# Kernel optimization log

Measured on AMD Instinct MI355X. Metric: run time of the kernel, lower is better.

## Reference

```python
import jax, jax.numpy as jnp
import numpy as np

B, T, N, F_IN = 8, 16, 1000, 16
E = 16000
H, D = 4, 32          # heads, gat_hidden_shape
HL = 64               # lstm hidden
OUT = 8
NEG_SLOPE = 0.2       # PyG GATConv default


def setup_inputs() -> dict:
    key = jax.random.key(0)
    ks = jax.random.split(key, 10)
    def init(k, shape, fan):
        return (jax.random.normal(k, shape, jnp.float32) / np.sqrt(fan)).astype(jnp.float32)
    x = jax.random.normal(ks[0], (B, T, N, F_IN), jnp.float32)
    edge_index = jax.random.randint(ks[1], (2, E), 0, N)
    W_gat = init(ks[2], (F_IN, H * D), F_IN)       # GATConv lin weight
    att_src = init(ks[3], (H, D), D)
    att_dst = init(ks[4], (H, D), D)
    b_gat = jnp.zeros((H * D,), jnp.float32)
    W_ih = init(ks[5], (4 * HL, H * D), H * D)     # LSTM, gate order i,f,g,o
    W_hh = init(ks[6], (4 * HL, HL), HL)
    b_ih = jnp.zeros((4 * HL,), jnp.float32)
    b_hh = jnp.zeros((4 * HL,), jnp.float32)
    W_clf = init(ks[7], (OUT, HL), HL)
    b_clf = jnp.zeros((OUT,), jnp.float32)
    return {"x": x, "edge_index": edge_index, "W_gat": W_gat, "att_src": att_src,
            "att_dst": att_dst, "b_gat": b_gat, "W_ih": W_ih, "W_hh": W_hh,
            "b_ih": b_ih, "b_hh": b_hh, "W_clf": W_clf, "b_clf": b_clf}


def reference(x, edge_index, W_gat, att_src, att_dst, b_gat,
              W_ih, W_hh, b_ih, b_hh, W_clf, b_clf):
    Bx, Tx, Nx, Fx = x.shape
    x_flat = x.reshape(Bx * Tx, Nx, Fx)
    # PyG GATConv adds self-loops by default
    loop = jnp.arange(Nx)
    src = jnp.concatenate([edge_index[0], loop])
    dst = jnp.concatenate([edge_index[1], loop])

    def gat_graph(xg):  # xg: [N, F]
        xp = (xg @ W_gat).reshape(Nx, H, D)                 # [N,H,D]
        a_s = jnp.einsum('nhd,hd->nh', xp, att_src)         # [N,H]
        a_d = jnp.einsum('nhd,hd->nh', xp, att_dst)
        e = jax.nn.leaky_relu(a_s[src] + a_d[dst], NEG_SLOPE)  # [E+N,H]
        m = jax.ops.segment_max(e, dst, num_segments=Nx)       # per-target softmax
        ex = jnp.exp(e - m[dst])
        denom = jax.ops.segment_sum(ex, dst, num_segments=Nx)
        alpha = ex / denom[dst]                                # [E+N,H]
        out = jax.ops.segment_sum(alpha[..., None] * xp[src], dst, num_segments=Nx)
        return out.reshape(Nx, H * D) + b_gat                  # [N, H*D]

    gat = jax.vmap(gat_graph)(x_flat)          # [B*T, N, H*D]
    gat = jax.nn.relu(gat)
    pooled = gat.max(axis=1)                   # global_max_pool -> [B*T, H*D]
    seq = pooled.reshape(Bx, Tx, H * D)

    h0 = jnp.zeros((Bx, HL), jnp.float32)
    c0 = jnp.zeros((Bx, HL), jnp.float32)

    def step(carry, xt):  # xt: [B, H*D]
        h, c = carry
        gates = xt @ W_ih.T + h @ W_hh.T + b_ih + b_hh
        i, f, g, o = jnp.split(gates, 4, axis=-1)
        i, f, o = jax.nn.sigmoid(i), jax.nn.sigmoid(f), jax.nn.sigmoid(o)
        g = jnp.tanh(g)
        c = f * c + i * g
        h = o * jnp.tanh(c)
        return (h, c), None

    (hT, _), _ = jax.lax.scan(step, (h0, c0), seq.transpose(1, 0, 2))
    return hT @ W_clf.T + b_clf                # [B, OUT]
```

## Files before the change

### kernel.cpp

```cpp
#include <hip/hip_runtime.h>
#include <hip/hip_bf16.h>
#include <stdint.h>

namespace {
constexpr int kB = 8, kT = 16, kN = 1000, kF = 16;
constexpr int kE = 16000;
constexpr int kH = 4, kHD = 128;
constexpr int kHL = 64, kOUT = 8;
constexpr int kG = kB * kT;
constexpr float kNeg = 0.2f;

constexpr size_t CX_WG   = 0;
constexpr size_t CX_ATS  = CX_WG   + 2048;
constexpr size_t CX_ATD  = CX_ATS  + 128;
constexpr size_t CX_BG   = CX_ATD  + 128;
constexpr size_t CX_WIH  = CX_BG   + 128;
constexpr size_t CX_WHH  = CX_WIH  + 32768;
constexpr size_t CX_BIH  = CX_WHH  + 16384;
constexpr size_t CX_BHH  = CX_BIH  + 256;
constexpr size_t CX_WCLF = CX_BHH  + 256;
constexpr size_t CX_BCLF = CX_WCLF + 512;
constexpr size_t CX_TOTAL = CX_BCLF + 8;

constexpr size_t OFF_FLAG  = 0;
constexpr size_t OFF_ROW   = 256;
constexpr size_t OFF_COL   = 4352;
constexpr size_t OFF_POOL  = 68608;
constexpr size_t OFF_CANON = 134400;
constexpr size_t OFF_AS    = 239872;
}

__device__ __forceinline__ float bf2f(unsigned short u) {
    return __uint_as_float(((uint32_t)u) << 16);
}
__device__ __forceinline__ float blo(uint32_t u) { return __uint_as_float(u << 16); }
__device__ __forceinline__ unsigned short f2bf(float f) {
    uint32_t u = __float_as_uint(f);
    uint32_t r = (u + 0x7fff + ((u >> 16) & 1)) >> 16;
    return (unsigned short)r;
}
__device__ __forceinline__ float sigm(float x) { return 1.f / (1.f + __expf(-x)); }

__device__ __forceinline__ int detect_isf(const unsigned short* xs, int t,
                                          int nthr, int* sh_cnt) {
    if (t == 0) *sh_cnt = 0;
    __syncthreads();
    int loc = 0;
    for (int i = t; i < 2048; i += nthr) {
        unsigned short u = xs[i];
        int ex = (u >> 7) & 0xff;
        if (u == 0 || (ex >= 97 && ex <= 143)) loc++;
    }
    atomicAdd(sh_cnt, loc);
    __syncthreads();
    return (*sh_cnt >= (2048 * 8) / 10) ? 0 : 1;
}

struct ConvArgs {
    const unsigned short* src[10];
    int n[10];
};

__global__ __launch_bounds__(256) void mega_setup(
        const void* __restrict__ xraw, const int* __restrict__ ei,
        ConvArgs ca,
        const unsigned short* __restrict__ WgR,
        const unsigned short* __restrict__ atsR,
        const unsigned short* __restrict__ atdR,
        int* __restrict__ flag, int* __restrict__ row, int* __restrict__ col,
        unsigned short* __restrict__ canon,
        unsigned short* __restrict__ xp_all,
        float* __restrict__ as_all, float* __restrict__ ad_all,
        unsigned int* __restrict__ pooled) {
    const int t = threadIdx.x;
    const unsigned short* xs = (const unsigned short*)xraw;

    if (blockIdx.x == 0) {
        __shared__ int cnt[1024];
        __shared__ int wtot[4];
        const int lane = t & 63, w = t >> 6;
        for (int i = t; i < 1024; i += 256) cnt[i] = 0;
        __syncthreads();
        const int* dst = ei + kE;
        for (int e = t; e < kE; e += 256) atomicAdd(&cnt[dst[e]], 1);
        __syncthreads();
        const int n0 = 4 * t;
        int c0 = cnt[n0], c1 = cnt[n0 + 1], c2 = cnt[n0 + 2], c3 = cnt[n0 + 3];
        int s0 = c0, s1 = s0 + c1, s2 = s1 + c2, s3 = s2 + c3;
        int tot = s3;
#pragma unroll
        for (int sft = 1; sft < 64; sft <<= 1) {
            int v = __shfl_up(tot, sft, 64);
            if (lane >= sft) tot += v;
        }
        if (lane == 63) wtot[w] = tot;
        __syncthreads();
        int wexcl = 0;
        for (int j = 0; j < w; ++j) wexcl += wtot[j];
        const int excl = wexcl + tot - s3;
        if (t == 0) row[0] = 0;
        if (n0 < kN) {
            row[n0 + 1] = excl + s0;
            row[n0 + 2] = excl + s1;
            row[n0 + 3] = excl + s2;
            row[n0 + 4] = excl + s3;
        }
        __syncthreads();
        cnt[n0] = excl; cnt[n0 + 1] = excl + s0;
        cnt[n0 + 2] = excl + s1; cnt[n0 + 3] = excl + s2;
        __syncthreads();
        for (int e = t; e < kE; e += 256) {
            int d0 = dst[e];
            int pos = atomicAdd(&cnt[d0], 1);
            col[pos] = ei[e];
        }
    } else if (blockIdx.x == 1) {
        __shared__ int dcnt;
        const int isf = detect_isf(xs, t, 256, &dcnt);
        if (t == 0) *flag = isf;
        size_t base = 0;
        for (int s = 0; s < 10; ++s) {
            const int n = ca.n[s];
            if (isf) {
                const float* fp = (const float*)ca.src[s];
                for (int i = t; i < n; i += 256) canon[base + i] = f2bf(fp[i]);
            } else {
                const unsigned short* sp = ca.src[s];
                for (int i = t; i < n; i += 256) canon[base + i] = sp[i];
            }
            base += (size_t)n;
        }
        for (int i = t; i < kG * kHD; i += 256) pooled[i] = 0u;
    } else {
        __shared__ int dcnt;
        __shared__ float Wl[kF * kHD];
        __shared__ float asl[kHD], adl[kHD];
        __shared__ float xr[64][kF];
        __shared__ float ws2[2][4][16];
        const int isf = detect_isf(xs, t, 256, &dcnt);
        const int i0 = blockIdx.x - 2;
        const int v = i0 & 7;
        const int jj = i0 >> 3;
        const int gl = v + 8 * (jj >> 4);
        const int nb = jj & 15;
        if (isf) {
            const float* wf = (const float*)WgR;
            for (int i = t; i < kF * kHD; i += 256) Wl[i] = wf[i];
            if (t < kHD) asl[t] = ((const float*)atsR)[t];
            else if (t < 2 * kHD) adl[t - kHD] = ((const float*)atdR)[t - kHD];
        } else {
            for (int i = t; i < kF * kHD; i += 256) Wl[i] = bf2f(WgR[i]);
            if (t < kHD) asl[t] = bf2f(atsR[t]);
            else if (t < 2 * kHD) adl[t - kHD] = bf2f(atdR[t - kHD]);
        }
        const int n0 = nb * 64;
        const int nn = min(64, kN - n0);
        const size_t xbase = (size_t)gl * kN * kF + (size_t)n0 * kF;
        if (isf) {
            const float* xf = (const float*)xraw;
            for (int i = t; i < nn * kF; i += 256) xr[i >> 4][i & 15] = xf[xbase + i];
        } else {
            for (int i = t; i < nn * kF; i += 256) xr[i >> 4][i & 15] = bf2f(xs[xbase + i]);
        }
        __syncthreads();

        if (t < 128) {
            const int sd = t >> 6, h = (t >> 4) & 3, f = t & 15;
            const float* att = sd ? adl : asl;
            float acc = 0.f;
#pragma unroll
            for (int d = 0; d < 32; ++d) acc += Wl[f * kHD + h * 32 + d] * att[h * 32 + d];
            ws2[sd][h][f] = acc;
        }

        unsigned short* xp = xp_all + (size_t)gl * kN * kHD;
        {
            const int c = t & 127;
            const int sub1 = t >> 7;
            float wreg[kF];
#pragma unroll
            for (int f = 0; f < kF; ++f) wreg[f] = Wl[f * kHD + c];
            for (int ln = sub1; ln < nn; ln += 2) {
                const float4* xrv = (const float4*)xr[ln];
                const float4 x0 = xrv[0], x1 = xrv[1], x2 = xrv[2], x3 = xrv[3];
                float vv = x0.x * wreg[0]  + x0.y * wreg[1]  + x0.z * wreg[2]  + x0.w * wreg[3]
                         + x1.x * wreg[4]  + x1.y * wreg[5]  + x1.z * wreg[6]  + x1.w * wreg[7]
                         + x2.x * wreg[8]  + x2.y * wreg[9]  + x2.z * wreg[10] + x2.w * wreg[11]
                         + x3.x * wreg[12] + x3.y * wreg[13] + x3.z * wreg[14] + x3.w * wreg[15];
                xp[(size_t)(n0 + ln) * kHD + c] = f2bf(vv);
            }
        }
        __syncthreads();

        {
            const int n = t >> 2, h = t & 3;
            if (n < nn) {
                const float* xv = xr[n];
                const float* wsv = ws2[0][h];
                const float* wdv = ws2[1][h];
                float accS = 0.f, accD = 0.f;
#pragma unroll
                for (int f = 0; f < kF; ++f) {
                    const float xf = xv[f];
                    accS += xf * wsv[f];
                    accD += xf * wdv[f];
                }
                as_all[((size_t)gl * kN + n0 + n) * kH + h] = accS;
                ad_all[((size_t)gl * kN + n0 + n) * kH + h] = accD;
            }
        }
    }
}

__global__ __launch_bounds__(256) void gat_aggregate(
        const int* __restrict__ row, const int* __restrict__ col,
        const unsigned short* __restrict__ xp,
        const float* __restrict__ a_s, const float* __restrict__ a_d,
        const unsigned short* __restrict__ bg,
        unsigned int* __restrict__ pooled) {
    __shared__ int   col_lds[4][64];
    __shared__ float p_lds[4][4][72];
    __shared__ float pm[4][kHD];

    const int w = threadIdx.x >> 6;
    const int lane = threadIdx.x & 63;
    const int sub = lane >> 4;
    const int cl = lane & 15;
    const int hh = cl >> 2;
    const int xcd = blockIdx.x & 7;
    const int j = blockIdx.x >> 3;
    const int gl = xcd + 8 * (j / 25);
    const int blk = j % 25;
    const size_t gn = (size_t)gl * kN;
    const char* xpcl = (const char*)(xp + gn * kHD) + cl * 16;
    const float4* as4 = (const float4*)a_s + gn;
    const float4* ad4 = (const float4*)a_d + gn;
    const uint32_t* bg32 = (const uint32_t*)bg;
    float bgv[8];
#pragma unroll
    for (int jb = 0; jb < 4; ++jb) {
        uint32_t u = bg32[cl * 4 + jb];
        bgv[2 * jb] = blo(u);
        bgv[2 * jb + 1] = __uint_as_float(u & 0xffff0000u);
    }
    float pool[8];
#pragma unroll
    for (int jb = 0; jb < 8; ++jb) pool[jb] = 0.f;

    for (int it = 0; it < 10; ++it) {
        const int n = blk * 40 + it * 4 + w;
        const int r0 = row[n];
        const int deg = row[n + 1] - r0;
        const int E = deg + 1;
        const float4 dv = ad4[n];
        float acc[8];
#pragma unroll
        for (int jb = 0; jb < 8; ++jb) acc[jb] = 0.f;
        float dh = 0.f;

        for (int base = 0; base < E; base += 64) {
            const int cnt = min(64, E - base);
            const int cntP = (cnt + 3) & ~3;
            if (lane < cntP) {
                const int eg = base + lane;
                const bool act = lane < cnt;
                const int s = (act && eg < deg) ? col[r0 + eg] : n;
                float p0 = 0.f, p1 = 0.f, p2 = 0.f, p3 = 0.f;
                if (act) {
                    const float4 av = as4[s];
                    float t0 = av.x + dv.x, t1 = av.y + dv.y;
                    float t2 = av.z + dv.z, t3 = av.w + dv.w;
                    t0 = t0 > 0.f ? t0 : kNeg * t0;
                    t1 = t1 > 0.f ? t1 : kNeg * t1;
                    t2 = t2 > 0.f ? t2 : kNeg * t2;
                    t3 = t3 > 0.f ? t3 : kNeg * t3;
                    p0 = __expf(t0); p1 = __expf(t1);
                    p2 = __expf(t2); p3 = __expf(t3);
                }
                col_lds[w][lane] = s << 8;
                p_lds[w][0][lane] = p0;
                p_lds[w][1][lane] = p1;
                p_lds[w][2][lane] = p2;
                p_lds[w][3][lane] = p3;
            }
            for (int e0 = 0; e0 < cntP; e0 += 4) {
                const int e = e0 + sub;
                const int off = col_lds[w][e];
                const float al = p_lds[w][hh][e];
                const uint4 u = *(const uint4*)(xpcl + off);
                acc[0] += al * blo(u.x); acc[1] += al * __uint_as_float(u.x);
                acc[2] += al * blo(u.y); acc[3] += al * __uint_as_float(u.y);
                acc[4] += al * blo(u.z); acc[5] += al * __uint_as_float(u.z);
                acc[6] += al * blo(u.w); acc[7] += al * __uint_as_float(u.w);
                dh += al;
            }
        }
#pragma unroll
        for (int jb = 0; jb < 8; ++jb) {
            acc[jb] += __shfl_xor(acc[jb], 16, 64);
            acc[jb] += __shfl_xor(acc[jb], 32, 64);
        }
        dh += __shfl_xor(dh, 16, 64);
        dh += __shfl_xor(dh, 32, 64);
        const float inv = 1.f / dh;
#pragma unroll
        for (int jb = 0; jb < 8; ++jb) {
            const float o = acc[jb] * inv + bgv[jb];
            pool[jb] = fmaxf(pool[jb], o > 0.f ? o : 0.f);
        }
    }
    if (sub == 0) {
#pragma unroll
        for (int jb = 0; jb < 8; ++jb) pm[w][cl * 8 + jb] = pool[jb];
    }
    __syncthreads();
    if (w == 0 && sub == 0) {
        const size_t gp = (size_t)gl * kHD;
#pragma unroll
        for (int jb = 0; jb < 8; ++jb) {
            const int c = cl * 8 + jb;
            float vmax = fmaxf(fmaxf(pm[0][c], pm[1][c]), fmaxf(pm[2][c], pm[3][c]));
            atomicMax(pooled + gp + c, __float_as_uint(vmax));
        }
    }
}

__global__ __launch_bounds__(256) void lstm_head(
        const float* __restrict__ pooled,
        const unsigned short* __restrict__ Wih,
        const unsigned short* __restrict__ Whh,
        const unsigned short* __restrict__ bih,
        const unsigned short* __restrict__ bhh,
        const unsigned short* __restrict__ Wclf,
        const unsigned short* __restrict__ bclf,
        const int* __restrict__ flag,
        void* __restrict__ out) {
    const int b = blockIdx.x;
    const int r = threadIdx.x;
    __shared__ float xt[kHD];
    __shared__ float hs[kHL];
    __shared__ float gates[4 * kHL];

    uint32_t wih[64];
    const uint32_t* pw = (const uint32_t*)(Wih + (size_t)r * kHD);
#pragma unroll
    for (int j = 0; j < 64; ++j) wih[j] = pw[j];
    uint32_t whh[32];
    const uint32_t* ph = (const uint32_t*)(Whh + (size_t)r * kHL);
#pragma unroll
    for (int j = 0; j < 32; ++j) whh[j] = ph[j];
    const float bias = bf2f(bih[r]) + bf2f(bhh[r]);

    float c_st = 0.f;
    if (r < kHL) hs[r] = 0.f;
    __syncthreads();

    for (int t = 0; t < kT; ++t) {
        if (r < kHD) xt[r] = pooled[((size_t)b * kT + t) * kHD + r];
        __syncthreads();
        float a0 = 0.f, a1 = 0.f, a2 = 0.f, a3 = 0.f;
#pragma unroll
        for (int j = 0; j < 64; j += 4) {
            uint32_t u0 = wih[j], u1 = wih[j + 1], u2 = wih[j + 2], u3 = wih[j + 3];
            a0 += blo(u0) * xt[2 * j + 0] + __uint_as_float(u0 & 0xffff0000u) * xt[2 * j + 1];
            a1 += blo(u1) * xt[2 * j + 2] + __uint_as_float(u1 & 0xffff0000u) * xt[2 * j + 3];
            a2 += blo(u2) * xt[2 * j + 4] + __uint_as_float(u2 & 0xffff0000u) * xt[2 * j + 5];
            a3 += blo(u3) * xt[2 * j + 6] + __uint_as_float(u3 & 0xffff0000u) * xt[2 * j + 7];
        }
#pragma unroll
        for (int j = 0; j < 32; j += 4) {
            uint32_t u0 = whh[j], u1 = whh[j + 1], u2 = whh[j + 2], u3 = whh[j + 3];
            a0 += blo(u0) * hs[2 * j + 0] + __uint_as_float(u0 & 0xffff0000u) * hs[2 * j + 1];
            a1 += blo(u1) * hs[2 * j + 2] + __uint_as_float(u1 & 0xffff0000u) * hs[2 * j + 3];
            a2 += blo(u2) * hs[2 * j + 4] + __uint_as_float(u2 & 0xffff0000u) * hs[2 * j + 5];
            a3 += blo(u3) * hs[2 * j + 6] + __uint_as_float(u3 & 0xffff0000u) * hs[2 * j + 7];
        }
        gates[r] = bias + (a0 + a1) + (a2 + a3);
        __syncthreads();
        if (r < kHL) {
            const float iv = sigm(gates[r]);
            const float fv = sigm(gates[kHL + r]);
            const float gv = tanhf(gates[2 * kHL + r]);
            const float ov = sigm(gates[3 * kHL + r]);
            c_st = fv * c_st + iv * gv;
            hs[r] = ov * tanhf(c_st);
        }
        __syncthreads();
    }
    if (r < kOUT) {
        float acc = bf2f(bclf[r]);
#pragma unroll
        for (int k = 0; k < kHL; ++k) acc += hs[k] * bf2f(Wclf[r * kHL + k]);
        if (*flag) ((float*)out)[b * kOUT + r] = acc;
        else ((__hip_bfloat16*)out)[b * kOUT + r] = __float2bfloat16(acc);
    }
}

extern "C" void kernel_launch(void* const* d_in, const int* in_sizes, int n_in,
                              void* d_out, int out_size, void* d_ws, size_t ws_size,
                              hipStream_t stream) {
    const int* ei = (const int*)d_in[1];

    char* ws = (char*)d_ws;
    int*            flag   = (int*)(ws + OFF_FLAG);
    int*            row    = (int*)(ws + OFF_ROW);
    int*            colv   = (int*)(ws + OFF_COL);
    unsigned int*   pooled = (unsigned int*)(ws + OFF_POOL);
    unsigned short* canon  = (unsigned short*)(ws + OFF_CANON);

    unsigned short* cBg   = canon + CX_BG;
    unsigned short* cWih  = canon + CX_WIH;
    unsigned short* cWhh  = canon + CX_WHH;
    unsigned short* cBih  = canon + CX_BIH;
    unsigned short* cBhh  = canon + CX_BHH;
    unsigned short* cWclf = canon + CX_WCLF;
    unsigned short* cBclf = canon + CX_BCLF;

    float*          a_s = (float*)(ws + OFF_AS);
    float*          a_d = (float*)(ws + OFF_AS + (size_t)kG * 16000);
    unsigned short* xp  = (unsigned short*)(ws + OFF_AS + (size_t)kG * 32000);

    ConvArgs ca;
    const int sizes[10] = {2048, 128, 128, 128, 32768, 16384, 256, 256, 512, 8};
    const int which[10] = {2, 3, 4, 5, 6, 7, 8, 9, 10, 11};
    for (int i = 0; i < 10; ++i) {
        ca.src[i] = (const unsigned short*)d_in[which[i]];
        ca.n[i] = sizes[i];
    }

    mega_setup<<<2 + kG * 16, 256, 0, stream>>>(
        d_in[0], ei, ca,
        (const unsigned short*)d_in[2], (const unsigned short*)d_in[3],
        (const unsigned short*)d_in[4],
        flag, row, colv, canon, xp, a_s, a_d, pooled);
    gat_aggregate<<<kG * 25, 256, 0, stream>>>(row, colv, xp, a_s, a_d, cBg, pooled);
    lstm_head<<<kB, 256, 0, stream>>>((const float*)pooled, cWih, cWhh, cBih, cBhh,
                                      cWclf, cBclf, flag, d_out);
}
```

Measured before the change: 226.2 us.

## Spread setup work over more blocks, pack bf16 stores, double aggregate grid

```diff
diff --git a/kernel.cpp b/kernel.cpp
--- a/kernel.cpp
+++ b/kernel.cpp
@@ -28,6 +28,8 @@
 constexpr size_t OFF_POOL  = 68608;
 constexpr size_t OFF_CANON = 134400;
 constexpr size_t OFF_AS    = 239872;
+
+constexpr int kSetupBlocks = 10;
 }
 
 __device__ __forceinline__ float bf2f(unsigned short u) {
@@ -114,31 +116,33 @@
             int pos = atomicAdd(&cnt[d0], 1);
             col[pos] = ei[e];
         }
-    } else if (blockIdx.x == 1) {
+    } else if (blockIdx.x <= 8) {
         __shared__ int dcnt;
         const int isf = detect_isf(xs, t, 256, &dcnt);
-        if (t == 0) *flag = isf;
+        if (blockIdx.x == 1 && t == 0) *flag = isf;
+        const int gid = (int)(blockIdx.x - 1) * 256 + t;
         size_t base = 0;
         for (int s = 0; s < 10; ++s) {
             const int n = ca.n[s];
             if (isf) {
                 const float* fp = (const float*)ca.src[s];
-                for (int i = t; i < n; i += 256) canon[base + i] = f2bf(fp[i]);
+                for (int i = gid; i < n; i += 2048) canon[base + i] = f2bf(fp[i]);
             } else {
                 const unsigned short* sp = ca.src[s];
-                for (int i = t; i < n; i += 256) canon[base + i] = sp[i];
+                for (int i = gid; i < n; i += 2048) canon[base + i] = sp[i];
             }
             base += (size_t)n;
         }
+    } else if (blockIdx.x == 9) {
         for (int i = t; i < kG * kHD; i += 256) pooled[i] = 0u;
     } else {
         __shared__ int dcnt;
         __shared__ float Wl[kF * kHD];
         __shared__ float asl[kHD], adl[kHD];
-        __shared__ float xr[64][kF];
+        __shared__ float xr[64][20];
         __shared__ float ws2[2][4][16];
         const int isf = detect_isf(xs, t, 256, &dcnt);
-        const int i0 = blockIdx.x - 2;
+        const int i0 = blockIdx.x - kSetupBlocks;
         const int v = i0 & 7;
         const int jj = i0 >> 3;
         const int gl = v + 8 * (jj >> 4);
@@ -167,27 +171,40 @@
         if (t < 128) {
             const int sd = t >> 6, h = (t >> 4) & 3, f = t & 15;
             const float* att = sd ? adl : asl;
+            const int d0r = t & 31;
             float acc = 0.f;
 #pragma unroll
-            for (int d = 0; d < 32; ++d) acc += Wl[f * kHD + h * 32 + d] * att[h * 32 + d];
+            for (int i = 0; i < 32; ++i) {
+                const int d = (d0r + i) & 31;
+                acc += Wl[f * kHD + h * 32 + d] * att[h * 32 + d];
+            }
             ws2[sd][h][f] = acc;
         }
 
-        unsigned short* xp = xp_all + (size_t)gl * kN * kHD;
+        uint32_t* xp32 = (uint32_t*)(xp_all + (size_t)gl * kN * kHD);
         {
-            const int c = t & 127;
-            const int sub1 = t >> 7;
-            float wreg[kF];
-#pragma unroll
-            for (int f = 0; f < kF; ++f) wreg[f] = Wl[f * kHD + c];
-            for (int ln = sub1; ln < nn; ln += 2) {
+            const int p = t & 63;
+            const int q = t >> 6;
+            const int c0 = 2 * p;
+            float wA[kF], wB[kF];
+#pragma unroll
+            for (int f = 0; f < kF; ++f) {
+                wA[f] = Wl[f * kHD + c0];
+                wB[f] = Wl[f * kHD + c0 + 1];
+            }
+            for (int ln = q; ln < nn; ln += 4) {
                 const float4* xrv = (const float4*)xr[ln];
                 const float4 x0 = xrv[0], x1 = xrv[1], x2 = xrv[2], x3 = xrv[3];
-                float vv = x0.x * wreg[0]  + x0.y * wreg[1]  + x0.z * wreg[2]  + x0.w * wreg[3]
-                         + x1.x * wreg[4]  + x1.y * wreg[5]  + x1.z * wreg[6]  + x1.w * wreg[7]
-                         + x2.x * wreg[8]  + x2.y * wreg[9]  + x2.z * wreg[10] + x2.w * wreg[11]
-                         + x3.x * wreg[12] + x3.y * wreg[13] + x3.z * wreg[14] + x3.w * wreg[15];
-                xp[(size_t)(n0 + ln) * kHD + c] = f2bf(vv);
+                float vA = x0.x * wA[0]  + x0.y * wA[1]  + x0.z * wA[2]  + x0.w * wA[3]
+                         + x1.x * wA[4]  + x1.y * wA[5]  + x1.z * wA[6]  + x1.w * wA[7]
+                         + x2.x * wA[8]  + x2.y * wA[9]  + x2.z * wA[10] + x2.w * wA[11]
+                         + x3.x * wA[12] + x3.y * wA[13] + x3.z * wA[14] + x3.w * wA[15];
+                float vB = x0.x * wB[0]  + x0.y * wB[1]  + x0.z * wB[2]  + x0.w * wB[3]
+                         + x1.x * wB[4]  + x1.y * wB[5]  + x1.z * wB[6]  + x1.w * wB[7]
+                         + x2.x * wB[8]  + x2.y * wB[9]  + x2.z * wB[10] + x2.w * wB[11]
+                         + x3.x * wB[12] + x3.y * wB[13] + x3.z * wB[14] + x3.w * wB[15];
+                const uint32_t pk = (uint32_t)f2bf(vA) | ((uint32_t)f2bf(vB) << 16);
+                xp32[(size_t)(n0 + ln) * 64 + p] = pk;
             }
         }
         __syncthreads();
@@ -229,8 +246,8 @@
     const int hh = cl >> 2;
     const int xcd = blockIdx.x & 7;
     const int j = blockIdx.x >> 3;
-    const int gl = xcd + 8 * (j / 25);
-    const int blk = j % 25;
+    const int gl = xcd + 8 * (j / 50);
+    const int blk = j % 50;
     const size_t gn = (size_t)gl * kN;
     const char* xpcl = (const char*)(xp + gn * kHD) + cl * 16;
     const float4* as4 = (const float4*)a_s + gn;
@@ -247,8 +264,8 @@
 #pragma unroll
     for (int jb = 0; jb < 8; ++jb) pool[jb] = 0.f;
 
-    for (int it = 0; it < 10; ++it) {
-        const int n = blk * 40 + it * 4 + w;
+    for (int it = 0; it < 5; ++it) {
+        const int n = blk * 20 + it * 4 + w;
         const int r0 = row[n];
         const int deg = row[n + 1] - r0;
         const int E = deg + 1;
@@ -428,12 +445,12 @@
         ca.n[i] = sizes[i];
     }
 
-    mega_setup<<<2 + kG * 16, 256, 0, stream>>>(
+    mega_setup<<<kSetupBlocks + kG * 16, 256, 0, stream>>>(
         d_in[0], ei, ca,
         (const unsigned short*)d_in[2], (const unsigned short*)d_in[3],
         (const unsigned short*)d_in[4],
         flag, row, colv, canon, xp, a_s, a_d, pooled);
-    gat_aggregate<<<kG * 25, 256, 0, stream>>>(row, colv, xp, a_s, a_d, cBg, pooled);
+    gat_aggregate<<<kG * 50, 256, 0, stream>>>(row, colv, xp, a_s, a_d, cBg, pooled);
     lstm_head<<<kB, 256, 0, stream>>>((const float*)pooled, cWih, cWhh, cBih, cBhh,
                                       cWclf, cBclf, flag, d_out);
 }
```

Result: slower. 251.0 us (+11.0%).
